# Kernel tuning notes

Measured on AMD Instinct MI355X. Metric: run time of the kernel, lower is better.

The kernel has to match this reference:

```python
import jax, jax.numpy as jnp
import numpy as np

D_MAX = 10

def setup_inputs() -> dict:
    key = jax.random.key(0)
    x = jax.random.normal(key, (2000000, 3), dtype=jnp.float32)
    return {"x": x}

def reference(x):
    # omega: [d] = 2^i frequencies
    omega = jnp.asarray(2.0 ** np.arange(D_MAX), dtype=x.dtype)
    # phase: [N, C, d]
    phase = x[:, :, None] * omega[None, None, :]
    # pe: [N, C, 2, d] with sin at index 0, cos at index 1 along axis 2
    pe = jnp.stack([jnp.sin(phase), jnp.cos(phase)], axis=2)
    return pe.reshape(x.shape[0], -1)
```

## Files before the change

### kernel.cpp

```cpp
#include <hip/hip_runtime.h>
#include <hip/hip_bf16.h>


#define ENC_BLOCK 192
#define ENC_PER 20

__global__ __launch_bounds__(ENC_BLOCK)
void Encoder_65077344469353_kernel(const float* __restrict__ x,
                                   float* __restrict__ out,
                                   int n_elem) {
    __shared__ float lds[ENC_BLOCK * ENC_PER];

    const int t = threadIdx.x;
    const long long base = (long long)blockIdx.x * ENC_BLOCK;
    const long long e = base + t;

    float xv = 0.0f;
    if (e < n_elem) xv = x[e];

    const float INV2PI = 0.15915494309189535f;
    float rv = xv * INV2PI;

    float* dst = &lds[t * ENC_PER];
    #pragma unroll
    for (int d = 0; d < 10; ++d) {
        float r = __builtin_amdgcn_fractf(rv);
        dst[d]      = __builtin_amdgcn_sinf(r);
        dst[10 + d] = __builtin_amdgcn_cosf(r);
        rv *= 2.0f;
    }
    __syncthreads();

    const long long out_base_f = base * ENC_PER;
    const long long out_total_f = (long long)n_elem * ENC_PER;
    const float4* lds4 = (const float4*)lds;
    float4* out4 = (float4*)(out + out_base_f);
    #pragma unroll
    for (int i = 0; i < 5; ++i) {
        int j = i * ENC_BLOCK + t;
        if (out_base_f + (long long)j * 4 < out_total_f)
            out4[j] = lds4[j];
    }
}

extern "C" void kernel_launch(void* const* d_in, const int* in_sizes, int n_in,
                              void* d_out, int out_size, void* d_ws, size_t ws_size,
                              hipStream_t stream) {
    const float* x = (const float*)d_in[0];
    float* out = (float*)d_out;
    const int n_elem = in_sizes[0];
    const int blocks = (n_elem + ENC_BLOCK - 1) / ENC_BLOCK;
    Encoder_65077344469353_kernel<<<dim3(blocks), dim3(ENC_BLOCK), 0, stream>>>(
        x, out, n_elem);
}
```

Measured before the change: 94.82 us.

## Assign one float4 output per thread and drop LDS staging

Each thread now computes one float4 of the output, five threads per input element, and stores it straight to global memory instead of staging a per-element row of 20 values in shared memory and copying it out after a barrier. Cosine is computed as sine of phase plus a quarter turn, and the power-of-two scale is built directly from exponent bits. This removes the LDS traffic and the synchronisation and raises thread count, at the cost of redundant loads of x and a per-thread integer divide by 5. Precision changes slightly because each phase is computed by one FMA from the original value rather than by repeated doubling, and cosine now comes from an offset sine.

```diff
diff --git a/kernel.cpp b/kernel.cpp
--- a/kernel.cpp
+++ b/kernel.cpp
@@ -2,45 +2,37 @@
 #include <hip/hip_bf16.h>
 
 
-#define ENC_BLOCK 192
-#define ENC_PER 20
+#define ENC_BLOCK 320
 
 __global__ __launch_bounds__(ENC_BLOCK)
 void Encoder_65077344469353_kernel(const float* __restrict__ x,
                                    float* __restrict__ out,
                                    int n_elem) {
-    __shared__ float lds[ENC_BLOCK * ENC_PER];
+    const long long nq = (long long)n_elem * 5;
+    const long long g  = (long long)blockIdx.x * ENC_BLOCK + threadIdx.x;
+    if (g >= nq) return;
 
-    const int t = threadIdx.x;
-    const long long base = (long long)blockIdx.x * ENC_BLOCK;
-    const long long e = base + t;
-
-    float xv = 0.0f;
-    if (e < n_elem) xv = x[e];
+    const unsigned g32 = (unsigned)g;
+    const unsigned e   = g32 / 5u;
+    const int      q   = (int)(g32 - e * 5u);
 
     const float INV2PI = 0.15915494309189535f;
-    float rv = xv * INV2PI;
+    const float rv = x[e] * INV2PI;
 
-    float* dst = &lds[t * ENC_PER];
+    float v[4];
     #pragma unroll
-    for (int d = 0; d < 10; ++d) {
-        float r = __builtin_amdgcn_fractf(rv);
-        dst[d]      = __builtin_amdgcn_sinf(r);
-        dst[10 + d] = __builtin_amdgcn_cosf(r);
-        rv *= 2.0f;
+    for (int i = 0; i < 4; ++i) {
+        const int s   = q * 4 + i;
+        const int isc = (s >= 10) ? 1 : 0;
+        const int d   = s - 10 * isc;
+        const float sc  = __uint_as_float((unsigned)(127 + d) << 23);
+        const float off = isc ? 0.25f : 0.0f;
+        const float r = __builtin_amdgcn_fractf(__builtin_fmaf(rv, sc, off));
+        v[i] = __builtin_amdgcn_sinf(r);
     }
-    __syncthreads();
 
-    const long long out_base_f = base * ENC_PER;
-    const long long out_total_f = (long long)n_elem * ENC_PER;
-    const float4* lds4 = (const float4*)lds;
-    float4* out4 = (float4*)(out + out_base_f);
-    #pragma unroll
-    for (int i = 0; i < 5; ++i) {
-        int j = i * ENC_BLOCK + t;
-        if (out_base_f + (long long)j * 4 < out_total_f)
-            out4[j] = lds4[j];
-    }
+    float4 o; o.x = v[0]; o.y = v[1]; o.z = v[2]; o.w = v[3];
+    reinterpret_cast<float4*>(out)[g] = o;
 }
 
 extern "C" void kernel_launch(void* const* d_in, const int* in_sizes, int n_in,
@@ -49,7 +41,8 @@
     const float* x = (const float*)d_in[0];
     float* out = (float*)d_out;
     const int n_elem = in_sizes[0];
-    const int blocks = (n_elem + ENC_BLOCK - 1) / ENC_BLOCK;
+    const long long nq = (long long)n_elem * 5;
+    const int blocks = (int)((nq + ENC_BLOCK - 1) / ENC_BLOCK);
     Encoder_65077344469353_kernel<<<dim3(blocks), dim3(ENC_BLOCK), 0, stream>>>(
         x, out, n_elem);
 }
```

Result: slower. 123.9 us (+30.7%).
